# Optimization experiments

Hardware: AMD Instinct MI355X
Metric: run time of the kernel (lower is better)

## Reference

```python
import jax, jax.numpy as jnp
import numpy as np

B, T, D_IN, H, L, OUT, S = 128, 256, 8, 512, 2, 2, 32
A = H  # attention_size == hidden_size


def lstm_cell(h, c, xt, Wih, Whh, b):
    # PyTorch LSTM gate order: i, f, g, o ; b = b_ih + b_hh (combined)
    g = xt @ Wih.T + h @ Whh.T + b
    i, f, gg, o = jnp.split(g, 4, axis=-1)
    c = jax.nn.sigmoid(f) * c + jax.nn.sigmoid(i) * jnp.tanh(gg)
    h = jax.nn.sigmoid(o) * jnp.tanh(c)
    return h, c


def setup_inputs() -> dict:
    key = jax.random.key(0)
    ks = jax.random.split(key, 20)
    w = lambda k, shape: jax.random.normal(k, shape, jnp.float32) * 0.1
    return {
        "x": jax.random.normal(ks[0], (B, T, D_IN), jnp.float32),
        # bidirectional encoder, 2 layers; leading dim 2 = (fwd, bwd)
        "enc_Wih0": w(ks[1], (2, 4 * H, D_IN)),
        "enc_Whh0": w(ks[2], (2, 4 * H, H)),
        "enc_b0": w(ks[3], (2, 4 * H)),
        "enc_Wih1": w(ks[4], (2, 4 * H, 2 * H)),
        "enc_Whh1": w(ks[5], (2, 4 * H, H)),
        "enc_b1": w(ks[6], (2, 4 * H)),
        # unidirectional decoder, 2 layers; layer0 input = output_size + 2H
        "dec_Wih0": w(ks[7], (4 * H, 2 * H + OUT)),
        "dec_Whh0": w(ks[8], (4 * H, H)),
        "dec_b0": w(ks[9], (4 * H,)),
        "dec_Wih1": w(ks[10], (4 * H, H)),
        "dec_Whh1": w(ks[11], (4 * H, H)),
        "dec_b1": w(ks[12], (4 * H,)),
        # Bahdanau attention (no biases)
        "Wa": w(ks[13], (A, 2 * H)),
        "Ua": w(ks[14], (A, H)),
        "Va": w(ks[15], (1, A)),
        "proj_W": w(ks[16], (H, H)),
        "proj_b": jnp.zeros((H,), jnp.float32),
        "fc_W": w(ks[17], (OUT, H)),
        "fc_b": jnp.zeros((OUT,), jnp.float32),
    }


def _forward(x, enc_Wih0, enc_Whh0, enc_b0, enc_Wih1, enc_Whh1, enc_b1,
             dec_Wih0, dec_Whh0, dec_b0, dec_Wih1, dec_Whh1, dec_b1,
             Wa, Ua, Va, proj_W, proj_b, fc_W, fc_b):
    Bb = x.shape[0]
    xT = jnp.swapaxes(x, 0, 1)  # [T,B,D]

    def run_dir(seq, Wih, Whh, b, reverse):
        h0 = jnp.zeros((Bb, H), x.dtype)
        def step(carry, xt):
            h, c = lstm_cell(carry[0], carry[1], xt, Wih, Whh, b)
            return (h, c), h
        (hT, cT), hs = jax.lax.scan(step, (h0, h0), seq, reverse=reverse)
        return hs, hT, cT

    # encoder layer 0 (bidirectional)
    of, hf0, cf0 = run_dir(xT, enc_Wih0[0], enc_Whh0[0], enc_b0[0], False)
    ob, hb0, cb0 = run_dir(xT, enc_Wih0[1], enc_Whh0[1], enc_b0[1], True)
    l1in = jnp.concatenate([of, ob], -1)  # [T,B,2H]
    # encoder layer 1
    of1, hf1, cf1 = run_dir(l1in, enc_Wih1[0], enc_Whh1[0], enc_b1[0], False)
    ob1, hb1, cb1 = run_dir(l1in, enc_Wih1[1], enc_Whh1[1], enc_b1[1], True)
    enc_out = jnp.swapaxes(jnp.concatenate([of1, ob1], -1), 0, 1)  # [B,T,2H]

    # torch hidden order: [l0_fwd, l0_bwd, l1_fwd, l1_bwd]; code takes first num_layers=2
    dh = jnp.tanh(jnp.stack([hf0, hb0]) @ proj_W.T + proj_b)  # [2,B,H]
    dc = jnp.stack([cf0, cb0])

    Wa_vals = enc_out @ Wa.T  # [B,T,A], loop-invariant part of attention
    y0 = x[:, -1, :OUT]

    def dec_step(carry, _):
        h, c, y = carry
        q = h[-1]  # [B,H] last-layer hidden
        score = jnp.tanh(Wa_vals + (q @ Ua.T)[:, None, :]) @ Va.T  # [B,T,1]
        wts = jax.nn.softmax(score, axis=1)
        z = jnp.sum(wts * enc_out, axis=1)  # [B,2H]
        h0n, c0n = lstm_cell(h[0], c[0], jnp.concatenate([y, z], 1), dec_Wih0, dec_Whh0, dec_b0)
        h1n, c1n = lstm_cell(h[1], c[1], h0n, dec_Wih1, dec_Whh1, dec_b1)
        yn = h1n @ fc_W.T + fc_b  # [B,OUT]
        return (jnp.stack([h0n, h1n]), jnp.stack([c0n, c1n]), yn), yn

    _, ys = jax.lax.scan(dec_step, (dh, dc, y0), None, length=S)
    return jnp.swapaxes(ys, 0, 1)  # [B,S,OUT]


def reference(x, enc_Wih0, enc_Whh0, enc_b0, enc_Wih1, enc_Whh1, enc_b1,
              dec_Wih0, dec_Whh0, dec_b0, dec_Wih1, dec_Whh1, dec_b1,
              Wa, Ua, Va, proj_W, proj_b, fc_W, fc_b):
    return _forward(x, enc_Wih0, enc_Whh0, enc_b0, enc_Wih1, enc_Whh1, enc_b1,
                    dec_Wih0, dec_Whh0, dec_b0, dec_Wih1, dec_Whh1, dec_b1,
                    Wa, Ua, Va, proj_W, proj_b, fc_W, fc_b)
```

## Files before the change

### kernel.cpp

```cpp
#include <hip/hip_runtime.h>

typedef _Float16 h16;
typedef __attribute__((ext_vector_type(8))) _Float16 f16x8;
typedef __attribute__((ext_vector_type(4))) float f32x4;

#define B_ 128
#define T_ 256
#define H_ 512
#define S_ 32

__device__ __forceinline__ float fexp2(float x){ return __builtin_amdgcn_exp2f(x); }
__device__ __forceinline__ float frcp (float x){ return __builtin_amdgcn_rcpf(x); }
__device__ __forceinline__ float fsig (float x){ return frcp(1.f + fexp2(-1.44269504089f*x)); }
__device__ __forceinline__ float ftanh(float x){ return 1.f - 2.f*frcp(1.f + fexp2(2.88539008178f*x)); }

struct StepArgs {
  const h16* X;  int sx; int Kx;
  const h16* Wih;
  const h16* Hp; int sh;
  const h16* Whh;
  const float* bias;
  float* C;
  h16* Hn; int shn;
};

__global__ __launch_bounds__(256) void lstm_step(StepArgs a0, StepArgs a1) {
  StepArgs A = (blockIdx.y == 0) ? a0 : a1;
  const int m0   = (blockIdx.x >> 5) << 4;
  const int j0   = (blockIdx.x & 31) << 4;
  const int wid  = threadIdx.x >> 6;
  const int lane = threadIdx.x & 63;
  const int r = lane & 15, g = lane >> 4;
  const int n0 = wid * H_ + j0;

  f32x4 acc = {0.f, 0.f, 0.f, 0.f};
  {
    const h16* xp = A.X   + (size_t)(m0 + r) * A.sx + g * 8;
    const h16* wp = A.Wih + (size_t)(n0 + r) * A.Kx + g * 8;
    for (int k = 0; k < A.Kx; k += 32) {
      f16x8 av = *(const f16x8*)(xp + k);
      f16x8 bv = *(const f16x8*)(wp + k);
      acc = __builtin_amdgcn_mfma_f32_16x16x32_f16(av, bv, acc, 0, 0, 0);
    }
  }
  {
    const h16* hp = A.Hp  + (size_t)(m0 + r) * A.sh + g * 8;
    const h16* wp = A.Whh + (size_t)(n0 + r) * H_   + g * 8;
    #pragma unroll
    for (int k = 0; k < H_; k += 32) {
      f16x8 av = *(const f16x8*)(hp + k);
      f16x8 bv = *(const f16x8*)(wp + k);
      acc = __builtin_amdgcn_mfma_f32_16x16x32_f16(av, bv, acc, 0, 0, 0);
    }
  }
  __shared__ float gt[4][16][16];
  #pragma unroll
  for (int t = 0; t < 4; ++t) gt[wid][g * 4 + t][r] = acc[t];
  __syncthreads();

  const int mi = threadIdx.x >> 4, ji = threadIdx.x & 15;
  const int jj = j0 + ji;
  float iv = gt[0][mi][ji] + A.bias[jj];
  float fv = gt[1][mi][ji] + A.bias[H_ + jj];
  float gv = gt[2][mi][ji] + A.bias[2 * H_ + jj];
  float ov = gt[3][mi][ji] + A.bias[3 * H_ + jj];
  float* cp = A.C + (size_t)(m0 + mi) * H_ + jj;
  float c = fsig(fv) * *cp + fsig(iv) * ftanh(gv);
  *cp = c;
  A.Hn[(size_t)(m0 + mi) * A.shn + jj] = (h16)(fsig(ov) * ftanh(c));
}

__global__ __launch_bounds__(256) void gemm_tn(const h16* Am, int lda, const h16* Bm,
                                               const float* bias, void* Cout, int ldc,
                                               int K, int mode) {
  const int wid = threadIdx.x >> 6, lane = threadIdx.x & 63;
  const int r = lane & 15, g = lane >> 4;
  const int m0 = (blockIdx.x * 4 + wid) * 16;
  const int n0 = blockIdx.y * 64;
  f32x4 acc[4] = {{0,0,0,0},{0,0,0,0},{0,0,0,0},{0,0,0,0}};
  const h16* ap = Am + (size_t)(m0 + r) * lda + g * 8;
  const h16* bp = Bm + (size_t)(n0 + r) * K + g * 8;
  for (int k = 0; k < K; k += 32) {
    f16x8 av = *(const f16x8*)(ap + k);
    #pragma unroll
    for (int j = 0; j < 4; ++j) {
      f16x8 bv = *(const f16x8*)(bp + (size_t)j * 16 * K + k);
      acc[j] = __builtin_amdgcn_mfma_f32_16x16x32_f16(av, bv, acc[j], 0, 0, 0);
    }
  }
  #pragma unroll
  for (int j = 0; j < 4; ++j) {
    const int n = n0 + j * 16 + r;
    const float badd = bias ? bias[n] : 0.f;
    #pragma unroll
    for (int t = 0; t < 4; ++t) {
      const int m = m0 + g * 4 + t;
      float v = acc[j][t] + badd;
      if (mode == 2) v = ftanh(v);
      if (mode == 0) ((float*)Cout)[(size_t)m * ldc + n] = v;
      else           ((h16*)Cout) [(size_t)m * ldc + n] = (h16)v;
    }
  }
}

__global__ __launch_bounds__(256) void attn_score(const h16* __restrict__ Wv,
                                                  const float* __restrict__ qUa,
                                                  const float* __restrict__ Va,
                                                  float* __restrict__ score) {
  const int wid = threadIdx.x >> 6, lane = threadIdx.x & 63;
  const int wv = blockIdx.x * 4 + wid;
  const int m = wv >> 8, t = wv & 255;
  const h16*  wrow = Wv + (size_t)(m * 256 + t) * 512;
  const float* qrow = qUa + m * 512;
  float s = 0.f;
  #pragma unroll
  for (int i = 0; i < 8; ++i) {
    const int a = i * 64 + lane;
    s += ftanh((float)wrow[a] + qrow[a]) * Va[a];
  }
  #pragma unroll
  for (int o = 32; o; o >>= 1) s += __shfl_xor(s, o);
  if (lane == 0) score[m * 256 + t] = s;
}

__global__ __launch_bounds__(256) void attn_ctx(const float* __restrict__ score,
                                                const h16* __restrict__ enc,
                                                h16* __restrict__ xcat) {
  const int m = blockIdx.x, tid = threadIdx.x;
  __shared__ float red[256];
  __shared__ float wts[256];
  const float s = score[m * 256 + tid];
  red[tid] = s; __syncthreads();
  for (int o = 128; o; o >>= 1) { if (tid < o) red[tid] = fmaxf(red[tid], red[tid + o]); __syncthreads(); }
  const float mx = red[0]; __syncthreads();
  const float p = fexp2((s - mx) * 1.44269504089f);
  red[tid] = p; __syncthreads();
  for (int o = 128; o; o >>= 1) { if (tid < o) red[tid] += red[tid + o]; __syncthreads(); }
  wts[tid] = p * frcp(red[0]);
  __syncthreads();
  const h16* erow = enc + (size_t)m * 256 * 1024;
  #pragma unroll
  for (int i = 0; i < 4; ++i) {
    const int k = i * 256 + tid;
    float a0 = 0, a1 = 0, a2 = 0, a3 = 0;
    for (int t = 0; t < 256; t += 4) {
      a0 += wts[t    ] * (float)erow[(t    ) * 1024 + k];
      a1 += wts[t + 1] * (float)erow[(t + 1) * 1024 + k];
      a2 += wts[t + 2] * (float)erow[(t + 2) * 1024 + k];
      a3 += wts[t + 3] * (float)erow[(t + 3) * 1024 + k];
    }
    xcat[(size_t)m * 1056 + 2 + k] = (h16)((a0 + a1) + (a2 + a3));
  }
}

__global__ __launch_bounds__(256) void fc_out(const h16* __restrict__ h1,
                                              const float* __restrict__ fcW,
                                              const float* __restrict__ fcb,
                                              float* __restrict__ outcol,
                                              h16* __restrict__ xcat) {
  const int wid = threadIdx.x >> 6, lane = threadIdx.x & 63;
  const int wv = blockIdx.x * 4 + wid;
  #pragma unroll
  for (int j = 0; j < 4; ++j) {
    const int idx = wv * 4 + j;
    const int m = idx >> 1, o = idx & 1;
    float s = 0.f;
    #pragma unroll
    for (int i = 0; i < 8; ++i) {
      const int k = i * 64 + lane;
      s += (float)h1[m * 512 + k] * fcW[o * 512 + k];
    }
    #pragma unroll
    for (int off = 32; off; off >>= 1) s += __shfl_xor(s, off);
    if (lane == 0) {
      const float y = s + fcb[o];
      outcol[m * (S_ * 2) + o] = y;
      xcat[(size_t)m * 1056 + o] = (h16)y;
    }
  }
}

__global__ void convert_pad(const float* __restrict__ in, h16* __restrict__ out,
                            int rows, int Kin, int Kout) {
  const size_t i = (size_t)blockIdx.x * 256 + threadIdx.x;
  if (i >= (size_t)rows * Kout) return;
  const int r = (int)(i / Kout), k = (int)(i % Kout);
  out[i] = (k < Kin) ? (h16)in[(size_t)r * Kin + k] : (h16)0.f;
}

__global__ void y0_init(const float* __restrict__ x, h16* __restrict__ xcat) {
  const int tid = threadIdx.x;
  if (tid < 256) {
    const int m = tid >> 1, o = tid & 1;
    xcat[(size_t)m * 1056 + o] = (h16)x[(size_t)(m * T_ + (T_ - 1)) * 8 + o];
  }
}

extern "C" void kernel_launch(void* const* d_in, const int* in_sizes, int n_in,
                              void* d_out, int out_size, void* d_ws, size_t ws_size,
                              hipStream_t stream) {
  const float* x     = (const float*)d_in[0];
  const float* eWih0 = (const float*)d_in[1];
  const float* eWhh0 = (const float*)d_in[2];
  const float* eb0   = (const float*)d_in[3];
  const float* eWih1 = (const float*)d_in[4];
  const float* eWhh1 = (const float*)d_in[5];
  const float* eb1   = (const float*)d_in[6];
  const float* dWih0 = (const float*)d_in[7];
  const float* dWhh0 = (const float*)d_in[8];
  const float* db0   = (const float*)d_in[9];
  const float* dWih1 = (const float*)d_in[10];
  const float* dWhh1 = (const float*)d_in[11];
  const float* db1   = (const float*)d_in[12];
  const float* Wa    = (const float*)d_in[13];
  const float* Ua    = (const float*)d_in[14];
  const float* Va    = (const float*)d_in[15];
  const float* projW = (const float*)d_in[16];
  const float* projb = (const float*)d_in[17];
  const float* fcW   = (const float*)d_in[18];
  const float* fcb   = (const float*)d_in[19];
  float* out = (float*)d_out;

  size_t cur = 0;
  auto alloc = [&](size_t bytes) {
    void* p = (char*)d_ws + cur;
    cur += (bytes + 255) & ~(size_t)255;
    return p;
  };
  h16*  zero   = (h16*) alloc((size_t)B_ * H_ * 2);
  h16*  xpad   = (h16*) alloc((size_t)B_ * T_ * 32 * 2);
  h16*  l1in   = (h16*) alloc((size_t)T_ * B_ * 1024 * 2);
  h16*  encout = (h16*) alloc((size_t)B_ * T_ * 1024 * 2);
  h16*  WaV    = (h16*) alloc((size_t)B_ * T_ * H_ * 2);
  float* cbuf  = (float*)alloc((size_t)4 * B_ * H_ * 4);
  float* c0 = cbuf;
  float* c1 = cbuf + 2 * B_ * H_;
  float* score = (float*)alloc((size_t)B_ * T_ * 4);
  float* qUa   = (float*)alloc((size_t)B_ * H_ * 4);
  h16*  xcat   = (h16*) alloc((size_t)B_ * 1056 * 2);
  h16*  dh0    = (h16*) alloc((size_t)2 * B_ * H_ * 2);
  h16*  dh1    = (h16*) alloc((size_t)2 * B_ * H_ * 2);
  h16*  bWih0  = (h16*) alloc((size_t)2 * 2048 * 32 * 2);
  h16*  bWhh0  = (h16*) alloc((size_t)2 * 2048 * 512 * 2);
  h16*  bWih1  = (h16*) alloc((size_t)2 * 2048 * 1024 * 2);
  h16*  bWhh1  = (h16*) alloc((size_t)2 * 2048 * 512 * 2);
  h16*  bdWih0 = (h16*) alloc((size_t)2048 * 1056 * 2);
  h16*  bdWhh0 = (h16*) alloc((size_t)2048 * 512 * 2);
  h16*  bdWih1 = (h16*) alloc((size_t)2048 * 512 * 2);
  h16*  bdWhh1 = (h16*) alloc((size_t)2048 * 512 * 2);
  h16*  bWa    = (h16*) alloc((size_t)512 * 1024 * 2);
  h16*  bUa    = (h16*) alloc((size_t)512 * 512 * 2);
  h16*  bprojW = (h16*) alloc((size_t)512 * 512 * 2);
  if (cur > ws_size) return;

  hipMemsetAsync(zero, 0, (size_t)B_ * H_ * 2, stream);
  hipMemsetAsync(cbuf, 0, (size_t)4 * B_ * H_ * 4, stream);
  hipMemsetAsync(xcat, 0, (size_t)B_ * 1056 * 2, stream);

  auto conv = [&](const float* in, h16* o, int rows, int kin, int kout) {
    const size_t total = (size_t)rows * kout;
    convert_pad<<<dim3((unsigned)((total + 255) / 256)), dim3(256), 0, stream>>>(in, o, rows, kin, kout);
  };
  conv(x,     xpad,   B_ * T_,  8,    32);
  conv(eWih0, bWih0,  2 * 2048, 8,    32);
  conv(eWhh0, bWhh0,  2 * 2048, 512,  512);
  conv(eWih1, bWih1,  2 * 2048, 1024, 1024);
  conv(eWhh1, bWhh1,  2 * 2048, 512,  512);
  conv(dWih0, bdWih0, 2048,     1026, 1056);
  conv(dWhh0, bdWhh0, 2048,     512,  512);
  conv(dWih1, bdWih1, 2048,     512,  512);
  conv(dWhh1, bdWhh1, 2048,     512,  512);
  conv(Wa,    bWa,    512,      1024, 1024);
  conv(Ua,    bUa,    512,      512,  512);
  conv(projW, bprojW, 512,      512,  512);

  for (int i = 0; i < T_; ++i) {
    const int tf = i, tb = T_ - 1 - i;
    StepArgs f{}, b{};
    f.X = xpad + tf * 32;  f.sx = T_ * 32;  f.Kx = 32;
    f.Wih = bWih0;
    f.Hp = i ? l1in + (size_t)(tf - 1) * B_ * 1024 : zero;  f.sh = i ? 1024 : H_;
    f.Whh = bWhh0;  f.bias = eb0;  f.C = c0;
    f.Hn = l1in + (size_t)tf * B_ * 1024;  f.shn = 1024;
    b.X = xpad + tb * 32;  b.sx = T_ * 32;  b.Kx = 32;
    b.Wih = bWih0 + 2048 * 32;
    b.Hp = i ? l1in + (size_t)(tb + 1) * B_ * 1024 + 512 : zero;  b.sh = i ? 1024 : H_;
    b.Whh = bWhh0 + (size_t)2048 * 512;  b.bias = eb0 + 2048;  b.C = c0 + B_ * H_;
    b.Hn = l1in + (size_t)tb * B_ * 1024 + 512;  b.shn = 1024;
    lstm_step<<<dim3(256, 2), dim3(256), 0, stream>>>(f, b);
  }
  for (int i = 0; i < T_; ++i) {
    const int tf = i, tb = T_ - 1 - i;
    StepArgs f{}, b{};
    f.X = l1in + (size_t)tf * B_ * 1024;  f.sx = 1024;  f.Kx = 1024;
    f.Wih = bWih1;
    f.Hp = i ? encout + (size_t)(tf - 1) * 1024 : zero;  f.sh = i ? T_ * 1024 : H_;
    f.Whh = bWhh1;  f.bias = eb1;  f.C = c1;
    f.Hn = encout + (size_t)tf * 1024;  f.shn = T_ * 1024;
    b.X = l1in + (size_t)tb * B_ * 1024;  b.sx = 1024;  b.Kx = 1024;
    b.Wih = bWih1 + (size_t)2048 * 1024;
    b.Hp = i ? encout + (size_t)(tb + 1) * 1024 + 512 : zero;  b.sh = i ? T_ * 1024 : H_;
    b.Whh = bWhh1 + (size_t)2048 * 512;  b.bias = eb1 + 2048;  b.C = c1 + B_ * H_;
    b.Hn = encout + (size_t)tb * 1024 + 512;  b.shn = T_ * 1024;
    lstm_step<<<dim3(256, 2), dim3(256), 0, stream>>>(f, b);
  }

  gemm_tn<<<dim3(B_ * T_ / 64, 8), dim3(256), 0, stream>>>(encout, 1024, bWa, nullptr, WaV, 512, 1024, 1);
  gemm_tn<<<dim3(B_ / 64, 8), dim3(256), 0, stream>>>(l1in + (size_t)(T_ - 1) * B_ * 1024, 1024,
                                                      bprojW, projb, dh0, 512, 512, 2);
  gemm_tn<<<dim3(B_ / 64, 8), dim3(256), 0, stream>>>(l1in + 512, 1024,
                                                      bprojW, projb, dh1, 512, 512, 2);
  y0_init<<<dim3(1), dim3(256), 0, stream>>>(x, xcat);

  float* dc0 = c0;
  float* dc1 = c0 + B_ * H_;

  int pp = 0;
  for (int s = 0; s < S_; ++s) {
    const int nx = pp ^ 1;
    h16* h0c = dh0 + (size_t)pp * B_ * H_;  h16* h0n = dh0 + (size_t)nx * B_ * H_;
    h16* h1c = dh1 + (size_t)pp * B_ * H_;  h16* h1n = dh1 + (size_t)nx * B_ * H_;

    gemm_tn<<<dim3(2, 8), dim3(256), 0, stream>>>(h1c, 512, bUa, nullptr, qUa, 512, 512, 0);
    attn_score<<<dim3(B_ * T_ / 4), dim3(256), 0, stream>>>(WaV, qUa, Va, score);
    attn_ctx<<<dim3(B_), dim3(256), 0, stream>>>(score, encout, xcat);

    StepArgs a{};
    a.X = xcat;  a.sx = 1056;  a.Kx = 1056;  a.Wih = bdWih0;
    a.Hp = h0c;  a.sh = 512;   a.Whh = bdWhh0;  a.bias = db0;
    a.C = dc0;   a.Hn = h0n;   a.shn = 512;
    lstm_step<<<dim3(256, 1), dim3(256), 0, stream>>>(a, a);

    StepArgs a2{};
    a2.X = h0n;  a2.sx = 512;  a2.Kx = 512;  a2.Wih = bdWih1;
    a2.Hp = h1c; a2.sh = 512;  a2.Whh = bdWhh1;  a2.bias = db1;
    a2.C = dc1;  a2.Hn = h1n;  a2.shn = 512;
    lstm_step<<<dim3(256, 1), dim3(256), 0, stream>>>(a2, a2);

    fc_out<<<dim3(16), dim3(256), 0, stream>>>(h1n, fcW, fcb, out + s * 2, xcat);
    pp = nx;
  }
}
```

Measured before the change: 11.98 ms.

## Replace per-timestep encoder launches with persistent kernel using LDS-resident weights and grid barriers

Replaces the 512 per-timestep lstm_step launches for the bidirectional encoder with one persistent kernel of 256 workgroups, 128 per direction. Each workgroup keeps its slice of the input and recurrent weights in LDS for the whole sequence and syncs with the other workgroups of its direction through an atomic-flag grid barrier after every step. The intent is to remove launch overhead and the repeated weight reloads from global memory on every step. Gate combination is done with lane shuffles instead of LDS. This depends on all 256 workgroups being co-resident, since the spin barrier would deadlock otherwise, and it adds barrier latency to every step.

```diff
diff --git a/kernel.cpp b/kernel.cpp
--- a/kernel.cpp
+++ b/kernel.cpp
@@ -13,6 +13,140 @@
 __device__ __forceinline__ float frcp (float x){ return __builtin_amdgcn_rcpf(x); }
 __device__ __forceinline__ float fsig (float x){ return frcp(1.f + fexp2(-1.44269504089f*x)); }
 __device__ __forceinline__ float ftanh(float x){ return 1.f - 2.f*frcp(1.f + fexp2(2.88539008178f*x)); }
+
+struct EncP {
+  const h16 *xpad, *Wih0, *Whh0, *Wih1, *Whh1;
+  const float *b0, *b1;
+  h16 *l1in, *encout;
+  float *cdump;
+  unsigned int* slots;
+};
+
+__device__ __forceinline__ void gridbar(unsigned int* slots, int myslot, int base,
+                                        int n, unsigned int ep, int tid) {
+  __syncthreads();
+  if (tid == 0) {
+    __builtin_amdgcn_fence(__ATOMIC_RELEASE, "agent");
+    __hip_atomic_store(&slots[(size_t)myslot * 32], ep, __ATOMIC_RELAXED, __HIP_MEMORY_SCOPE_AGENT);
+  }
+  bool ok;
+  do {
+    ok = (tid < n) ? (__hip_atomic_load(&slots[(size_t)(base + tid) * 32],
+                                        __ATOMIC_RELAXED, __HIP_MEMORY_SCOPE_AGENT) >= ep)
+                   : true;
+  } while (!__syncthreads_and(ok));
+  if (tid == 0) __builtin_amdgcn_fence(__ATOMIC_ACQUIRE, "agent");
+  __syncthreads();
+}
+
+__global__ __launch_bounds__(512, 1) void encoder_persist(EncP P) {
+  const int wg = blockIdx.x, dir = wg >> 7;
+  const int j0 = (wg & 127) << 2;
+  const int tid = threadIdx.x, wid = tid >> 6, lane = tid & 63;
+  const int col = lane & 15, rowg = lane >> 4;
+  const int u = col & 3, gt = col >> 2;
+  const int m0 = wid << 4;
+
+  __shared__ h16 W[16][1544];
+
+  auto stage = [&](const h16* Wih, int Kx, const h16* Whh) {
+    const int CX = Kx >> 3, CT = CX + 64;
+    for (int i = tid; i < 16 * CT; i += 512) {
+      const int r = i / CT, c = i - r * CT;
+      const int grow = (r >> 2) * 512 + j0 + (r & 3);
+      f16x8 v = (c < CX) ? *(const f16x8*)(Wih + (size_t)grow * Kx + (c << 3))
+                         : *(const f16x8*)(Whh + (size_t)grow * 512 + ((c - CX) << 3));
+      *(f16x8*)(&W[r][c << 3]) = v;
+    }
+  };
+  auto pick = [&](float own, float p4, float p8, float p12, int x) {
+    return x == 0 ? own : x == 1 ? p4 : x == 2 ? p8 : p12;
+  };
+
+  unsigned int ep = 0;
+  float c0_ = 0.f, c1_ = 0.f, c2_ = 0.f, c3_ = 0.f;
+  float h0, h1, h2, h3;
+
+#define GATECOMB(av_, cvar, hvar, bias_)                                        \
+  { float a_ = av_ + bias_;                                                     \
+    float p4_ = __shfl_xor(a_, 4), p8_ = __shfl_xor(a_, 8), p12_ = __shfl_xor(a_, 12); \
+    float iv = pick(a_, p4_, p8_, p12_, gt);                                    \
+    float fv = pick(a_, p4_, p8_, p12_, gt ^ 1);                                \
+    float gv = pick(a_, p4_, p8_, p12_, gt ^ 2);                                \
+    float ov = pick(a_, p4_, p8_, p12_, gt ^ 3);                                \
+    cvar = fsig(fv) * cvar + fsig(iv) * ftanh(gv);                              \
+    hvar = fsig(ov) * ftanh(cvar); }
+
+  stage(P.Wih0 + (size_t)dir * 2048 * 32, 32, P.Whh0 + (size_t)dir * 2048 * 512);
+  const float bias0 = P.b0[dir * 2048 + gt * 512 + j0 + u];
+  __syncthreads();
+
+  for (int i = 0; i < 256; ++i) {
+    const int t = dir ? 255 - i : i;
+    f32x4 acc = {0.f, 0.f, 0.f, 0.f};
+    {
+      f16x8 av = *(const f16x8*)(P.xpad + ((size_t)(m0 + col) * T_ + t) * 32 + rowg * 8);
+      f16x8 bv = *(const f16x8*)(&W[col][rowg * 8]);
+      acc = __builtin_amdgcn_mfma_f32_16x16x32_f16(av, bv, acc, 0, 0, 0);
+    }
+    if (i) {
+      const int tp = dir ? t + 1 : t - 1;
+      const h16* ah = P.l1in + ((size_t)tp * B_ + m0 + col) * 1024 + dir * 512 + rowg * 8;
+      #pragma unroll
+      for (int ks = 0; ks < 16; ++ks) {
+        f16x8 av = *(const f16x8*)(ah + ks * 32);
+        f16x8 bv = *(const f16x8*)(&W[col][32 + ks * 32 + rowg * 8]);
+        acc = __builtin_amdgcn_mfma_f32_16x16x32_f16(av, bv, acc, 0, 0, 0);
+      }
+    }
+    GATECOMB(acc[0], c0_, h0, bias0) GATECOMB(acc[1], c1_, h1, bias0)
+    GATECOMB(acc[2], c2_, h2, bias0) GATECOMB(acc[3], c3_, h3, bias0)
+    const float hw = (gt == 0) ? h0 : (gt == 1) ? h1 : (gt == 2) ? h2 : h3;
+    const int bm = m0 + (rowg << 2) + gt;
+    P.l1in[((size_t)t * B_ + bm) * 1024 + dir * 512 + j0 + u] = (h16)hw;
+    gridbar(P.slots, wg, dir << 7, 128, ++ep, tid);
+  }
+  {
+    const float cw = (gt == 0) ? c0_ : (gt == 1) ? c1_ : (gt == 2) ? c2_ : c3_;
+    const int bm = m0 + (rowg << 2) + gt;
+    P.cdump[(size_t)dir * B_ * H_ + (size_t)bm * H_ + j0 + u] = cw;
+  }
+  gridbar(P.slots, wg, 0, 256, ++ep, tid);
+
+  stage(P.Wih1 + (size_t)dir * 2048 * 1024, 1024, P.Whh1 + (size_t)dir * 2048 * 512);
+  const float bias1 = P.b1[dir * 2048 + gt * 512 + j0 + u];
+  c0_ = c1_ = c2_ = c3_ = 0.f;
+  __syncthreads();
+
+  for (int i = 0; i < 256; ++i) {
+    const int t = dir ? 255 - i : i;
+    f32x4 acc = {0.f, 0.f, 0.f, 0.f};
+    const h16* ax = P.l1in + ((size_t)t * B_ + m0 + col) * 1024 + rowg * 8;
+    #pragma unroll
+    for (int ks = 0; ks < 32; ++ks) {
+      f16x8 av = *(const f16x8*)(ax + ks * 32);
+      f16x8 bv = *(const f16x8*)(&W[col][ks * 32 + rowg * 8]);
+      acc = __builtin_amdgcn_mfma_f32_16x16x32_f16(av, bv, acc, 0, 0, 0);
+    }
+    if (i) {
+      const int tp = dir ? t + 1 : t - 1;
+      const h16* ah = P.encout + ((size_t)(m0 + col) * T_ + tp) * 1024 + dir * 512 + rowg * 8;
+      #pragma unroll
+      for (int ks = 0; ks < 16; ++ks) {
+        f16x8 av = *(const f16x8*)(ah + ks * 32);
+        f16x8 bv = *(const f16x8*)(&W[col][1024 + ks * 32 + rowg * 8]);
+        acc = __builtin_amdgcn_mfma_f32_16x16x32_f16(av, bv, acc, 0, 0, 0);
+      }
+    }
+    GATECOMB(acc[0], c0_, h0, bias1) GATECOMB(acc[1], c1_, h1, bias1)
+    GATECOMB(acc[2], c2_, h2, bias1) GATECOMB(acc[3], c3_, h3, bias1)
+    const float hw = (gt == 0) ? h0 : (gt == 1) ? h1 : (gt == 2) ? h2 : h3;
+    const int bm = m0 + (rowg << 2) + gt;
+    P.encout[((size_t)bm * T_ + t) * 1024 + dir * 512 + j0 + u] = (h16)hw;
+    gridbar(P.slots, wg, dir << 7, 128, ++ep, tid);
+  }
+#undef GATECOMB
+}
 
 struct StepArgs {
   const h16* X;  int sx; int Kx;
@@ -24,8 +158,7 @@
   h16* Hn; int shn;
 };
 
-__global__ __launch_bounds__(256) void lstm_step(StepArgs a0, StepArgs a1) {
-  StepArgs A = (blockIdx.y == 0) ? a0 : a1;
+__global__ __launch_bounds__(256) void lstm_step(StepArgs A) {
   const int m0   = (blockIdx.x >> 5) << 4;
   const int j0   = (blockIdx.x & 31) << 4;
   const int wid  = threadIdx.x >> 6;
@@ -53,17 +186,17 @@
       acc = __builtin_amdgcn_mfma_f32_16x16x32_f16(av, bv, acc, 0, 0, 0);
     }
   }
-  __shared__ float gt[4][16][16];
-  #pragma unroll
-  for (int t = 0; t < 4; ++t) gt[wid][g * 4 + t][r] = acc[t];
+  __shared__ float gtl[4][16][16];
+  #pragma unroll
+  for (int t = 0; t < 4; ++t) gtl[wid][g * 4 + t][r] = acc[t];
   __syncthreads();
 
   const int mi = threadIdx.x >> 4, ji = threadIdx.x & 15;
   const int jj = j0 + ji;
-  float iv = gt[0][mi][ji] + A.bias[jj];
-  float fv = gt[1][mi][ji] + A.bias[H_ + jj];
-  float gv = gt[2][mi][ji] + A.bias[2 * H_ + jj];
-  float ov = gt[3][mi][ji] + A.bias[3 * H_ + jj];
+  float iv = gtl[0][mi][ji] + A.bias[jj];
+  float fv = gtl[1][mi][ji] + A.bias[H_ + jj];
+  float gv = gtl[2][mi][ji] + A.bias[2 * H_ + jj];
+  float ov = gtl[3][mi][ji] + A.bias[3 * H_ + jj];
   float* cp = A.C + (size_t)(m0 + mi) * H_ + jj;
   float c = fsig(fv) * *cp + fsig(iv) * ftanh(gv);
   *cp = c;
@@ -227,19 +360,17 @@
     cur += (bytes + 255) & ~(size_t)255;
     return p;
   };
-  h16*  zero   = (h16*) alloc((size_t)B_ * H_ * 2);
   h16*  xpad   = (h16*) alloc((size_t)B_ * T_ * 32 * 2);
   h16*  l1in   = (h16*) alloc((size_t)T_ * B_ * 1024 * 2);
   h16*  encout = (h16*) alloc((size_t)B_ * T_ * 1024 * 2);
   h16*  WaV    = (h16*) alloc((size_t)B_ * T_ * H_ * 2);
-  float* cbuf  = (float*)alloc((size_t)4 * B_ * H_ * 4);
-  float* c0 = cbuf;
-  float* c1 = cbuf + 2 * B_ * H_;
+  float* cdump = (float*)alloc((size_t)2 * B_ * H_ * 4);
   float* score = (float*)alloc((size_t)B_ * T_ * 4);
   float* qUa   = (float*)alloc((size_t)B_ * H_ * 4);
   h16*  xcat   = (h16*) alloc((size_t)B_ * 1056 * 2);
   h16*  dh0    = (h16*) alloc((size_t)2 * B_ * H_ * 2);
   h16*  dh1    = (h16*) alloc((size_t)2 * B_ * H_ * 2);
+  unsigned int* slots = (unsigned int*)alloc((size_t)256 * 32 * 4);
   h16*  bWih0  = (h16*) alloc((size_t)2 * 2048 * 32 * 2);
   h16*  bWhh0  = (h16*) alloc((size_t)2 * 2048 * 512 * 2);
   h16*  bWih1  = (h16*) alloc((size_t)2 * 2048 * 1024 * 2);
@@ -253,9 +384,8 @@
   h16*  bprojW = (h16*) alloc((size_t)512 * 512 * 2);
   if (cur > ws_size) return;
 
-  hipMemsetAsync(zero, 0, (size_t)B_ * H_ * 2, stream);
-  hipMemsetAsync(cbuf, 0, (size_t)4 * B_ * H_ * 4, stream);
-  hipMemsetAsync(xcat, 0, (size_t)B_ * 1056 * 2, stream);
+  (void)hipMemsetAsync(slots, 0, (size_t)256 * 32 * 4, stream);
+  (void)hipMemsetAsync(xcat, 0, (size_t)B_ * 1056 * 2, stream);
 
   auto conv = [&](const float* in, h16* o, int rows, int kin, int kout) {
     const size_t total = (size_t)rows * kout;
@@ -274,36 +404,10 @@
   conv(Ua,    bUa,    512,      512,  512);
   conv(projW, bprojW, 512,      512,  512);
 
-  for (int i = 0; i < T_; ++i) {
-    const int tf = i, tb = T_ - 1 - i;
-    StepArgs f{}, b{};
-    f.X = xpad + tf * 32;  f.sx = T_ * 32;  f.Kx = 32;
-    f.Wih = bWih0;
-    f.Hp = i ? l1in + (size_t)(tf - 1) * B_ * 1024 : zero;  f.sh = i ? 1024 : H_;
-    f.Whh = bWhh0;  f.bias = eb0;  f.C = c0;
-    f.Hn = l1in + (size_t)tf * B_ * 1024;  f.shn = 1024;
-    b.X = xpad + tb * 32;  b.sx = T_ * 32;  b.Kx = 32;
-    b.Wih = bWih0 + 2048 * 32;
-    b.Hp = i ? l1in + (size_t)(tb + 1) * B_ * 1024 + 512 : zero;  b.sh = i ? 1024 : H_;
-    b.Whh = bWhh0 + (size_t)2048 * 512;  b.bias = eb0 + 2048;  b.C = c0 + B_ * H_;
-    b.Hn = l1in + (size_t)tb * B_ * 1024 + 512;  b.shn = 1024;
-    lstm_step<<<dim3(256, 2), dim3(256), 0, stream>>>(f, b);
-  }
-  for (int i = 0; i < T_; ++i) {
-    const int tf = i, tb = T_ - 1 - i;
-    StepArgs f{}, b{};
-    f.X = l1in + (size_t)tf * B_ * 1024;  f.sx = 1024;  f.Kx = 1024;
-    f.Wih = bWih1;
-    f.Hp = i ? encout + (size_t)(tf - 1) * 1024 : zero;  f.sh = i ? T_ * 1024 : H_;
-    f.Whh = bWhh1;  f.bias = eb1;  f.C = c1;
-    f.Hn = encout + (size_t)tf * 1024;  f.shn = T_ * 1024;
-    b.X = l1in + (size_t)tb * B_ * 1024;  b.sx = 1024;  b.Kx = 1024;
-    b.Wih = bWih1 + (size_t)2048 * 1024;
-    b.Hp = i ? encout + (size_t)(tb + 1) * 1024 + 512 : zero;  b.sh = i ? T_ * 1024 : H_;
-    b.Whh = bWhh1 + (size_t)2048 * 512;  b.bias = eb1 + 2048;  b.C = c1 + B_ * H_;
-    b.Hn = encout + (size_t)tb * 1024 + 512;  b.shn = T_ * 1024;
-    lstm_step<<<dim3(256, 2), dim3(256), 0, stream>>>(f, b);
-  }
+  EncP P;
+  P.xpad = xpad; P.Wih0 = bWih0; P.Whh0 = bWhh0; P.Wih1 = bWih1; P.Whh1 = bWhh1;
+  P.b0 = eb0; P.b1 = eb1; P.l1in = l1in; P.encout = encout; P.cdump = cdump; P.slots = slots;
+  encoder_persist<<<dim3(256), dim3(512), 0, stream>>>(P);
 
   gemm_tn<<<dim3(B_ * T_ / 64, 8), dim3(256), 0, stream>>>(encout, 1024, bWa, nullptr, WaV, 512, 1024, 1);
   gemm_tn<<<dim3(B_ / 64, 8), dim3(256), 0, stream>>>(l1in + (size_t)(T_ - 1) * B_ * 1024, 1024,
@@ -312,8 +416,8 @@
                                                       bprojW, projb, dh1, 512, 512, 2);
   y0_init<<<dim3(1), dim3(256), 0, stream>>>(x, xcat);
 
-  float* dc0 = c0;
-  float* dc1 = c0 + B_ * H_;
+  float* dc0 = cdump;
+  float* dc1 = cdump + B_ * H_;
 
   int pp = 0;
   for (int s = 0; s < S_; ++s) {
@@ -329,13 +433,13 @@
     a.X = xcat;  a.sx = 1056;  a.Kx = 1056;  a.Wih = bdWih0;
     a.Hp = h0c;  a.sh = 512;   a.Whh = bdWhh0;  a.bias = db0;
     a.C = dc0;   a.Hn = h0n;   a.shn = 512;
-    lstm_step<<<dim3(256, 1), dim3(256), 0, stream>>>(a, a);
+    lstm_step<<<dim3(256), dim3(256), 0, stream>>>(a);
 
     StepArgs a2{};
     a2.X = h0n;  a2.sx = 512;  a2.Kx = 512;  a2.Wih = bdWih1;
     a2.Hp = h1c; a2.sh = 512;  a2.Whh = bdWhh1;  a2.bias = db1;
     a2.C = dc1;  a2.Hn = h1n;  a2.shn = 512;
-    lstm_step<<<dim3(256, 1), dim3(256), 0, stream>>>(a2, a2);
+    lstm_step<<<dim3(256), dim3(256), 0, stream>>>(a2);
 
     fc_out<<<dim3(16), dim3(256), 0, stream>>>(h1n, fcW, fcb, out + s * 2, xcat);
     pp = nx;
```

New measurement: 12.20 ms. Within noise of the previous version (+1.8%).
